# Kernel tuning notes

Hardware: AMD Instinct MI355X
Metric: run time of the kernel (lower is better)

The kernel has to match this reference:

```python
import jax, jax.numpy as jnp
import numpy as np
import math

B, S, H = 2, 2048, 2048
NH, HD = 16, 128
THETA = 10000.0
NEG = -1e9


def make_rope_tables(seq_len, head_dim, theta):
    inv_freq = 1.0 / (theta ** (np.arange(0, head_dim, 2, dtype=np.float32) / head_dim))
    pos = np.arange(seq_len, dtype=np.float32)
    freqs = np.outer(pos, inv_freq)                    # (S, HD/2)
    emb = np.concatenate([freqs, freqs], axis=-1)      # (S, HD)
    return jnp.asarray(np.cos(emb)), jnp.asarray(np.sin(emb))


def setup_inputs() -> dict:
    key = jax.random.key(0)
    k1, k2, k3 = jax.random.split(key, 3)
    hidden_states = jax.random.normal(k1, (B, S, H), dtype=jnp.float32)
    rope_cos, rope_sin = make_rope_tables(S, HD, THETA)
    # additive causal mask [1,1,S,S]
    causal = jnp.tril(jnp.ones((S, S), dtype=bool))
    attention_mask = jnp.where(causal, 0.0, NEG).astype(jnp.float32)[None, None]
    w_qkv = jax.random.normal(k2, (3 * H, H), dtype=jnp.float32) * (1.0 / math.sqrt(H))
    w_o = jax.random.normal(k3, (H, H), dtype=jnp.float32) * (1.0 / math.sqrt(H))
    return {"hidden_states": hidden_states, "rope_cos": rope_cos, "rope_sin": rope_sin,
            "attention_mask": attention_mask, "w_qkv": w_qkv, "w_o": w_o}


def apply_rope(x, cos, sin):
    # x: (B, NH, S, HD); cos/sin: (S, HD)
    half = x.shape[-1] // 2
    x1, x2 = x[..., :half], x[..., half:]
    x_rot = jnp.concatenate([-x2, x1], axis=-1)
    return x * cos[None, None] + x_rot * sin[None, None]


def reference(hidden_states, rope_cos, rope_sin, attention_mask, w_qkv, w_o):
    b, s, h = hidden_states.shape
    qkv = hidden_states @ w_qkv.T                      # (B, S, 3H)
    qkv = qkv.reshape(b, s, 3, NH, HD).transpose(2, 0, 3, 1, 4)  # (3, B, NH, S, HD)
    q, k, v = qkv[0], qkv[1], qkv[2]
    q = apply_rope(q, rope_cos, rope_sin)
    k = apply_rope(k, rope_cos, rope_sin)
    scale = 1.0 / math.sqrt(HD)
    scores = jnp.einsum('bhqd,bhkd->bhqk', q, k) * scale + attention_mask
    probs = jax.nn.softmax(scores.astype(jnp.float32), axis=-1).astype(q.dtype)
    out = jnp.einsum('bhqk,bhkd->bhqd', probs, v)      # (B, NH, S, HD)
    out = out.transpose(0, 2, 1, 3).reshape(b, s, h)
    return out @ w_o.T
```

## Files before the change

kernel.cpp:

```cpp
#include <hip/hip_runtime.h>
#include <stdint.h>

typedef unsigned int u32;
typedef unsigned short u16;

typedef __bf16 bf16x8 __attribute__((ext_vector_type(8)));
typedef float f32x4 __attribute__((ext_vector_type(4)));

struct alignas(16) V16 { u32 a, b, c, d; };

__device__ __forceinline__ u16 f2bf(float x) {
    u32 u = __float_as_uint(x);
    u += 0x7FFFu + ((u >> 16) & 1u);
    return (u16)(u >> 16);
}
__device__ __forceinline__ float bf2f(u16 h) {
    return __uint_as_float(((u32)h) << 16);
}

__device__ __forceinline__ bf16x8 ld_frag(const u16* p) {
    return __builtin_bit_cast(bf16x8, *(const V16*)p);
}

__device__ __forceinline__ void async_cp16(u16* lds_dst, const u16* g_src) {
    __builtin_amdgcn_global_load_lds(
        (__attribute__((address_space(1))) void*)g_src,
        (__attribute__((address_space(3))) void*)lds_dst, 16, 0, 0);
}

__global__ __launch_bounds__(256) void cast_all_kernel(
    const float* __restrict__ hidden, const float* __restrict__ wqkv,
    const float* __restrict__ wo,
    u16* __restrict__ hA, u16* __restrict__ wqb, u16* __restrict__ wob)
{
    int i = blockIdx.x * 256 + threadIdx.x;
    const float* src; u16* dst; int off;
    if (i < 2097152)      { src = hidden; dst = hA;  off = i; }
    else if (i < 5242880) { src = wqkv;   dst = wqb; off = i - 2097152; }
    else                  { src = wo;     dst = wob; off = i - 5242880; }
    const float* p = src + (size_t)off * 4;
    ushort4 o;
    o.x = f2bf(p[0]); o.y = f2bf(p[1]); o.z = f2bf(p[2]); o.w = f2bf(p[3]);
    *(ushort4*)(dst + (size_t)off * 4) = o;
}

__global__ __launch_bounds__(256) void gemm_bt(
    const u16* __restrict__ A, const u16* __restrict__ Bt,
    int M, int N, int K, int mode,
    float* __restrict__ Cout,
    u16* __restrict__ Qb, u16* __restrict__ Kb, u16* __restrict__ Vtb)
{
    __shared__ u16 smem[17408];
    u16* As = smem;
    u16* Bs = smem + 8192;

    const int t = threadIdx.x;
    const int w = t >> 6, l = t & 63;
    const int lr = l & 15;
    const int lk = (l >> 4) * 8;

    const int flat = blockIdx.y * gridDim.x + blockIdx.x;
    const int xcd = flat & 7, slot = flat >> 3;
    const int cpx = gridDim.x >> 3;
    const int ncol = xcd * cpx + slot % cpx;
    const int mrow = slot / cpx;
    const int m0 = mrow * 128, n0 = ncol * 128;
    const int wm = (w >> 1) * 64, wn = (w & 1) * 64;

    f32x4 acc[4][4];
#pragma unroll
    for (int i = 0; i < 4; ++i)
#pragma unroll
        for (int j = 0; j < 4; ++j) acc[i][j] = f32x4{0.f, 0.f, 0.f, 0.f};

    const u16* Ag = A + (size_t)m0 * K;
    const u16* Bg = Bt + (size_t)n0 * K;
    const int srow = l >> 2;
    const int scol = (l & 3) * 8;

    for (int k0 = 0; k0 < K; k0 += 64) {
#pragma unroll
        for (int g = 0; g < 2; ++g) {
            const int row = w * 32 + g * 16;
#pragma unroll
            for (int c = 0; c < 2; ++c) {
                async_cp16(&As[c * 4096 + row * 32],
                           Ag + (size_t)(row + srow) * K + k0 + c * 32 + scol);
                async_cp16(&Bs[c * 4096 + row * 32],
                           Bg + (size_t)(row + srow) * K + k0 + c * 32 + scol);
            }
        }
        __syncthreads();

#pragma unroll
        for (int c = 0; c < 2; ++c) {
            bf16x8 af[4], bf[4];
#pragma unroll
            for (int i = 0; i < 4; ++i)
                af[i] = ld_frag(&As[c * 4096 + (wm + i * 16 + lr) * 32 + lk]);
#pragma unroll
            for (int j = 0; j < 4; ++j)
                bf[j] = ld_frag(&Bs[c * 4096 + (wn + j * 16 + lr) * 32 + lk]);
#pragma unroll
            for (int i = 0; i < 4; ++i)
#pragma unroll
                for (int j = 0; j < 4; ++j)
                    acc[i][j] = __builtin_amdgcn_mfma_f32_16x16x32_bf16(af[i], bf[j], acc[i][j], 0, 0, 0);
        }
        __syncthreads();
    }

    const int lrow4 = (l >> 4) * 4;
    if (mode == 1) {
#pragma unroll
        for (int i = 0; i < 4; ++i)
#pragma unroll
            for (int j = 0; j < 4; ++j)
#pragma unroll
                for (int r = 0; r < 4; ++r) {
                    int gr = m0 + wm + i * 16 + lrow4 + r;
                    int gc = n0 + wn + j * 16 + lr;
                    Cout[(size_t)gr * N + gc] = acc[i][j][r];
                }
    } else {
        const int which = n0 >> 11;
        const int nh = (n0 & 2047) >> 7;
        const int bb = m0 >> 11;
        const int s0 = m0 & 2047;
        u16* Cs = smem;
        if (which < 2) {
#pragma unroll
            for (int i = 0; i < 4; ++i)
#pragma unroll
                for (int j = 0; j < 4; ++j)
#pragma unroll
                    for (int r = 0; r < 4; ++r)
                        Cs[(wm + i * 16 + lrow4 + r) * 136 + wn + j * 16 + lr] =
                            f2bf(acc[i][j][r]);
        } else {
#pragma unroll
            for (int i = 0; i < 4; ++i)
#pragma unroll
                for (int j = 0; j < 4; ++j)
#pragma unroll
                    for (int r = 0; r < 4; ++r)
                        Cs[(wn + j * 16 + lr) * 136 + wm + i * 16 + lrow4 + r] =
                            f2bf(acc[i][j][r]);
        }
        __syncthreads();
        const int rrow = t >> 4, rcol = (t & 15) * 8;
        if (which < 2) {
            u16* dst = (which == 0 ? Qb : Kb) +
                       ((size_t)(bb * 16 + nh) * 2048 + s0) * 128;
#pragma unroll
            for (int it = 0; it < 8; ++it) {
                int row = it * 16 + rrow;
                *(V16*)&dst[(size_t)row * 128 + rcol] = *(const V16*)&Cs[row * 136 + rcol];
            }
        } else {
            u16* dst = Vtb + (size_t)(bb * 16 + nh) * 128 * 2048 + s0;
#pragma unroll
            for (int it = 0; it < 8; ++it) {
                int d = it * 16 + rrow;
                *(V16*)&dst[(size_t)d * 2048 + rcol] = *(const V16*)&Cs[d * 136 + rcol];
            }
        }
    }
}

__global__ __launch_bounds__(256) void rope_kernel(
    u16* __restrict__ Qb, u16* __restrict__ Kb,
    const float* __restrict__ cosT, const float* __restrict__ sinT, float qscale)
{
    int idx = blockIdx.x * 256 + threadIdx.x;
    int d = (idx & 7) * 8;
    int s = (idx >> 3) & 2047;
    int bh = idx >> 14;
    size_t base = ((size_t)bh * 2048 + s) * 128;
    float c[8], sn[8];
#pragma unroll
    for (int i = 0; i < 8; ++i) {
        c[i]  = cosT[s * 128 + d + i];
        sn[i] = sinT[s * 128 + d + i];
    }
    union U { V16 v; u16 h[8]; };
    U qlo, qhi, klo, khi, a, bq, ak, bk;
    qlo.v = *(const V16*)&Qb[base + d];
    qhi.v = *(const V16*)&Qb[base + d + 64];
    klo.v = *(const V16*)&Kb[base + d];
    khi.v = *(const V16*)&Kb[base + d + 64];
#pragma unroll
    for (int i = 0; i < 8; ++i) {
        float q1 = bf2f(qlo.h[i]), q2 = bf2f(qhi.h[i]);
        a.h[i]  = f2bf((q1 * c[i] - q2 * sn[i]) * qscale);
        bq.h[i] = f2bf((q2 * c[i] + q1 * sn[i]) * qscale);
        float k1 = bf2f(klo.h[i]), k2 = bf2f(khi.h[i]);
        ak.h[i] = f2bf(k1 * c[i] - k2 * sn[i]);
        bk.h[i] = f2bf(k2 * c[i] + k1 * sn[i]);
    }
    *(V16*)&Qb[base + d]      = a.v;
    *(V16*)&Qb[base + d + 64] = bq.v;
    *(V16*)&Kb[base + d]      = ak.v;
    *(V16*)&Kb[base + d + 64] = bk.v;
}

#define PS_LD 72
__global__ __launch_bounds__(256, 2) void flash_attn(
    const u16* __restrict__ Qb, const u16* __restrict__ Kb, const u16* __restrict__ Vtb,
    u16* __restrict__ ctx)
{
    __shared__ u16 Ks[4 * 64 * 32];
    __shared__ u16 Vts[2 * 128 * 32];
    __shared__ u16 Ps[4 * 16 * PS_LD];

    const int t = threadIdx.x, w = t >> 6, l = t & 63;
    const int lr = l & 15, lk = (l >> 4) * 8, lrow4 = (l >> 4) * 4;
    const int bh = blockIdx.x;
    const int pidx = blockIdx.y;
    const int wm = w * 16;

    const u16* Qg = Qb + (size_t)bh * 2048 * 128;
    const u16* Kg = Kb + (size_t)bh * 2048 * 128;
    const u16* Vg = Vtb + (size_t)bh * 128 * 2048;
    u16* Pw = &Ps[w * 16 * PS_LD];

    const int srow = l >> 2;
    const int scol = (l & 3) * 8;
    const int vh = w & 1, vkc = w >> 1;

    const int b = bh >> 4, nh = bh & 15;

#pragma unroll
    for (int half = 0; half < 2; ++half) {
        const int qt = half ? pidx : 31 - pidx;
        const int q0 = qt * 64;

        bf16x8 qfrag[4];
#pragma unroll
        for (int kc = 0; kc < 4; ++kc)
            qfrag[kc] = ld_frag(&Qg[(size_t)(q0 + wm + lr) * 128 + kc * 32 + lk]);

        f32x4 oacc[8];
#pragma unroll
        for (int jo = 0; jo < 8; ++jo) oacc[jo] = f32x4{0.f, 0.f, 0.f, 0.f};
        float l_part[4] = {0.f, 0.f, 0.f, 0.f};

        const int ktiles = qt + 1;
        for (int kt = 0; kt < ktiles; ++kt) {
            const int c0 = kt * 64;
#pragma unroll
            for (int it = 0; it < 4; ++it)
                async_cp16(&Ks[w * 2048 + it * 512],
                           Kg + (size_t)(c0 + it * 16 + srow) * 128 + w * 32 + scol);
#pragma unroll
            for (int it = 0; it < 4; ++it)
                async_cp16(&Vts[vkc * 4096 + (vh * 64 + it * 16) * 32],
                           Vg + (size_t)(vh * 64 + it * 16 + srow) * 2048 + c0 + vkc * 32 + scol);
            __syncthreads();

            f32x4 pacc[4];
#pragma unroll
            for (int j = 0; j < 4; ++j) pacc[j] = f32x4{0.f, 0.f, 0.f, 0.f};
#pragma unroll
            for (int kc = 0; kc < 4; ++kc) {
                bf16x8 bk[4];
#pragma unroll
                for (int j = 0; j < 4; ++j)
                    bk[j] = ld_frag(&Ks[kc * 2048 + (j * 16 + lr) * 32 + lk]);
#pragma unroll
                for (int j = 0; j < 4; ++j)
                    pacc[j] = __builtin_amdgcn_mfma_f32_16x16x32_bf16(qfrag[kc], bk[j], pacc[j], 0, 0, 0);
            }

            if (kt == qt) {
#pragma unroll
                for (int j = 0; j < 4; ++j) {
                    const int cl = j * 16 + lr;
#pragma unroll
                    for (int r = 0; r < 4; ++r) {
                        float pv = (cl > wm + lrow4 + r) ? 0.f : __expf(pacc[j][r]);
                        pacc[j][r] = pv;
                        l_part[r] += pv;
                    }
                }
            } else {
#pragma unroll
                for (int j = 0; j < 4; ++j)
#pragma unroll
                    for (int r = 0; r < 4; ++r) {
                        float pv = __expf(pacc[j][r]);
                        pacc[j][r] = pv;
                        l_part[r] += pv;
                    }
            }

#pragma unroll
            for (int j = 0; j < 4; ++j)
#pragma unroll
                for (int r = 0; r < 4; ++r)
                    Pw[(lrow4 + r) * PS_LD + j * 16 + lr] = f2bf(pacc[j][r]);

#pragma unroll
            for (int kc = 0; kc < 2; ++kc) {
                bf16x8 ap = ld_frag(&Pw[lr * PS_LD + kc * 32 + lk]);
#pragma unroll
                for (int jo = 0; jo < 8; ++jo) {
                    bf16x8 bv = ld_frag(&Vts[kc * 4096 + (jo * 16 + lr) * 32 + lk]);
                    oacc[jo] = __builtin_amdgcn_mfma_f32_16x16x32_bf16(ap, bv, oacc[jo], 0, 0, 0);
                }
            }
            __syncthreads();
        }

        float linv[4];
#pragma unroll
        for (int r = 0; r < 4; ++r) {
            float s = l_part[r];
#pragma unroll
            for (int dd = 8; dd >= 1; dd >>= 1) s += __shfl_xor(s, dd);
            linv[r] = __builtin_amdgcn_rcpf(s);
        }
#pragma unroll
        for (int jo = 0; jo < 8; ++jo)
#pragma unroll
            for (int r = 0; r < 4; ++r) {
                int srow2 = q0 + wm + lrow4 + r;
                int col = nh * 128 + jo * 16 + lr;
                ctx[((size_t)b * 2048 + srow2) * 2048 + col] = f2bf(oacc[jo][r] * linv[r]);
            }
    }
}

extern "C" void kernel_launch(void* const* d_in, const int* in_sizes, int n_in,
                              void* d_out, int out_size, void* d_ws, size_t ws_size,
                              hipStream_t stream)
{
    (void)in_sizes; (void)n_in; (void)out_size; (void)ws_size;
    const float* hidden = (const float*)d_in[0];
    const float* cosT   = (const float*)d_in[1];
    const float* sinT   = (const float*)d_in[2];
    const float* wqkv   = (const float*)d_in[4];
    const float* wo     = (const float*)d_in[5];
    float* out = (float*)d_out;
    char* ws = (char*)d_ws;

    u16* hA   = (u16*)(ws + 0);
    u16* wqb  = (u16*)(ws + 16777216);
    u16* wob  = (u16*)(ws + 41943040);
    u16* Qb   = (u16*)(ws + 50331648);
    u16* Kb   = (u16*)(ws + 67108864);
    u16* Vtb  = (u16*)(ws + 83886080);
    u16* ctx  = (u16*)(ws + 100663296);

    cast_all_kernel<<<dim3(24576), dim3(256), 0, stream>>>(hidden, wqkv, wo,
                                                           hA, wqb, wob);

    gemm_bt<<<dim3(48, 32), dim3(256), 0, stream>>>(hA, wqb, 4096, 6144, 2048, 0,
                                                    nullptr, Qb, Kb, Vtb);
    rope_kernel<<<dim3(2048), dim3(256), 0, stream>>>(Qb, Kb, cosT, sinT,
                                                      0.08838834764831845f);

    flash_attn<<<dim3(32, 16), dim3(256), 0, stream>>>(Qb, Kb, Vtb, ctx);

    gemm_bt<<<dim3(16, 32), dim3(256), 0, stream>>>(ctx, wob, 4096, 2048, 2048, 1,
                                                    out, nullptr, nullptr, nullptr);
}
```

Measured before the change: 398.6 us.

## Pipeline GEMMs with double-buffered LDS, fuse RoPE epilogue, swizzle attention LDS

Replaces the GEMM with a 512-thread, 256x128-tile kernel. It double-buffers half-K LDS stages and overlaps async global loads with MFMA work using vmcnt waits, raw barriers and setprio. LDS reads are XOR-swizzled to avoid bank conflicts. RoPE and the Q scale move into the QKV GEMM epilogue, which removes the separate rope kernel and its read-modify-write pass over Q and K. The flash attention K/V LDS layouts are also changed to swizzled full-row tiles. The cost is more LDS per block (96KB dynamic), hand-tuned waitcnt logic that is fragile, and fewer blocks for the output GEMM.

```diff
diff --git a/kernel.cpp b/kernel.cpp
--- a/kernel.cpp
+++ b/kernel.cpp
@@ -44,73 +44,141 @@
     *(ushort4*)(dst + (size_t)off * 4) = o;
 }
 
-__global__ __launch_bounds__(256) void gemm_bt(
+__device__ __forceinline__ void stage_A(
+    u16* smem, const u16* __restrict__ Ag, int K,
+    int kk, int buf, int tile, int w, int rg0, int chl)
+{
+    u16* base = smem + buf * 16384 + kk * 8192;
+    const int kcol = tile * 64 + kk * 32 + chl * 8;
+#pragma unroll
+    for (int i = 0; i < 2; ++i) {
+        const int s = i * 8 + w;
+        async_cp16(base + s * 512, Ag + (size_t)(s * 16 + rg0) * K + kcol);
+    }
+}
+__device__ __forceinline__ void stage_B(
+    u16* smem, const u16* __restrict__ Bg, int K,
+    int kk, int buf, int tile, int w, int rg0, int chl)
+{
+    u16* base = smem + 32768 + buf * 8192 + kk * 4096;
+    const int kcol = tile * 64 + kk * 32 + chl * 8;
+    async_cp16(base + w * 512, Bg + (size_t)(w * 16 + rg0) * K + kcol);
+}
+
+__global__ __launch_bounds__(512, 2) void gemm_mn(
     const u16* __restrict__ A, const u16* __restrict__ Bt,
     int M, int N, int K, int mode,
     float* __restrict__ Cout,
-    u16* __restrict__ Qb, u16* __restrict__ Kb, u16* __restrict__ Vtb)
-{
-    __shared__ u16 smem[17408];
-    u16* As = smem;
-    u16* Bs = smem + 8192;
-
+    u16* __restrict__ Qb, u16* __restrict__ Kb, u16* __restrict__ Vtb,
+    const float* __restrict__ cosT, const float* __restrict__ sinT, float qscale)
+{
+    extern __shared__ u16 smem[];
     const int t = threadIdx.x;
     const int w = t >> 6, l = t & 63;
-    const int lr = l & 15;
-    const int lk = (l >> 4) * 8;
+    const int lr = l & 15, lk = (l >> 4) * 8;
+    const int wmr = w >> 1, wnc = w & 1;
+    const int wmr4 = wmr * 4, wnc4 = wnc * 4;
+    const int laneoff = lr * 32 + (lk ^ ((lr & 8) ? 16 : 0));
+    const int rg0 = l >> 2;
+    const int chl = (l & 3) ^ ((l >> 4) & 2);
 
     const int flat = blockIdx.y * gridDim.x + blockIdx.x;
     const int xcd = flat & 7, slot = flat >> 3;
     const int cpx = gridDim.x >> 3;
     const int ncol = xcd * cpx + slot % cpx;
     const int mrow = slot / cpx;
-    const int m0 = mrow * 128, n0 = ncol * 128;
-    const int wm = (w >> 1) * 64, wn = (w & 1) * 64;
-
-    f32x4 acc[4][4];
-#pragma unroll
-    for (int i = 0; i < 4; ++i)
-#pragma unroll
-        for (int j = 0; j < 4; ++j) acc[i][j] = f32x4{0.f, 0.f, 0.f, 0.f};
+    const int m0 = mrow * 256, n0 = ncol * 128;
 
     const u16* Ag = A + (size_t)m0 * K;
     const u16* Bg = Bt + (size_t)n0 * K;
-    const int srow = l >> 2;
-    const int scol = (l & 3) * 8;
-
-    for (int k0 = 0; k0 < K; k0 += 64) {
-#pragma unroll
-        for (int g = 0; g < 2; ++g) {
-            const int row = w * 32 + g * 16;
-#pragma unroll
-            for (int c = 0; c < 2; ++c) {
-                async_cp16(&As[c * 4096 + row * 32],
-                           Ag + (size_t)(row + srow) * K + k0 + c * 32 + scol);
-                async_cp16(&Bs[c * 4096 + row * 32],
-                           Bg + (size_t)(row + srow) * K + k0 + c * 32 + scol);
-            }
-        }
-        __syncthreads();
-
-#pragma unroll
-        for (int c = 0; c < 2; ++c) {
-            bf16x8 af[4], bf[4];
+
+    f32x4 acc[4][4];
+#pragma unroll
+    for (int i = 0; i < 4; ++i)
+#pragma unroll
+        for (int j = 0; j < 4; ++j) acc[i][j] = f32x4{0.f, 0.f, 0.f, 0.f};
+
+    const int NT = K >> 6;
+
+    stage_A(smem, Ag, K, 0, 0, 0, w, rg0, chl);
+    stage_B(smem, Bg, K, 0, 0, 0, w, rg0, chl);
+    stage_A(smem, Ag, K, 1, 0, 0, w, rg0, chl);
+    stage_B(smem, Bg, K, 1, 0, 0, w, rg0, chl);
+    stage_A(smem, Ag, K, 0, 1, 1, w, rg0, chl);
+    stage_B(smem, Bg, K, 0, 1, 1, w, rg0, chl);
+    asm volatile("s_waitcnt vmcnt(6)" ::: "memory");
+    __builtin_amdgcn_s_barrier();
+
+    bf16x8 af0[4], bf0[4], af1[4], bf1[4];
+#pragma unroll
+    for (int i = 0; i < 4; ++i)
+        af0[i] = ld_frag(smem + (wmr4 + i) * 512 + laneoff);
+#pragma unroll
+    for (int j = 0; j < 4; ++j)
+        bf0[j] = ld_frag(smem + 32768 + (wnc4 + j) * 512 + laneoff);
+
+    for (int tt = 0; tt < NT; ++tt) {
+        const int bsel = tt & 1;
+        const u16* Ab  = smem + bsel * 16384;
+        const u16* Bb  = smem + 32768 + bsel * 8192;
+        const u16* AbN = smem + (bsel ^ 1) * 16384;
+        const u16* BbN = smem + 32768 + (bsel ^ 1) * 8192;
+
+        if (tt + 1 < NT) {
+            stage_A(smem, Ag, K, 1, bsel ^ 1, tt + 1, w, rg0, chl);
+            stage_B(smem, Bg, K, 1, bsel ^ 1, tt + 1, w, rg0, chl);
+        }
+        if (tt < NT - 1) asm volatile("s_waitcnt vmcnt(6)" ::: "memory");
+        else             asm volatile("s_waitcnt vmcnt(0)" ::: "memory");
+        __builtin_amdgcn_s_barrier();
+        __builtin_amdgcn_s_setprio(1);
+#pragma unroll
+        for (int i = 0; i < 4; ++i)
+            af1[i] = ld_frag(Ab + 8192 + (wmr4 + i) * 512 + laneoff);
+#pragma unroll
+        for (int j = 0; j < 4; ++j)
+            bf1[j] = ld_frag(Bb + 4096 + (wnc4 + j) * 512 + laneoff);
+        __builtin_amdgcn_sched_barrier(0);
+#pragma unroll
+        for (int i = 0; i < 4; ++i)
+#pragma unroll
+            for (int j = 0; j < 4; ++j)
+                acc[i][j] = __builtin_amdgcn_mfma_f32_16x16x32_bf16(
+                    af0[i], bf0[j], acc[i][j], 0, 0, 0);
+        __builtin_amdgcn_s_setprio(0);
+        __builtin_amdgcn_s_barrier();
+
+        if (tt + 2 < NT) {
+            stage_A(smem, Ag, K, 0, bsel, tt + 2, w, rg0, chl);
+            stage_B(smem, Bg, K, 0, bsel, tt + 2, w, rg0, chl);
+        }
+        if (tt < NT - 2)       asm volatile("s_waitcnt vmcnt(6)" ::: "memory");
+        else if (tt == NT - 2) asm volatile("s_waitcnt vmcnt(3)" ::: "memory");
+        __builtin_amdgcn_s_barrier();
+        __builtin_amdgcn_s_setprio(1);
+        if (tt + 1 < NT) {
 #pragma unroll
             for (int i = 0; i < 4; ++i)
-                af[i] = ld_frag(&As[c * 4096 + (wm + i * 16 + lr) * 32 + lk]);
-#pragma unroll
-            for (int j = 0; j < 4; ++j)
-                bf[j] = ld_frag(&Bs[c * 4096 + (wn + j * 16 + lr) * 32 + lk]);
-#pragma unroll
-            for (int i = 0; i < 4; ++i)
-#pragma unroll
-                for (int j = 0; j < 4; ++j)
-                    acc[i][j] = __builtin_amdgcn_mfma_f32_16x16x32_bf16(af[i], bf[j], acc[i][j], 0, 0, 0);
-        }
-        __syncthreads();
-    }
-
+                af0[i] = ld_frag(AbN + (wmr4 + i) * 512 + laneoff);
+#pragma unroll
+            for (int j = 0; j < 4; ++j)
+                bf0[j] = ld_frag(BbN + (wnc4 + j) * 512 + laneoff);
+        }
+        __builtin_amdgcn_sched_barrier(0);
+#pragma unroll
+        for (int i = 0; i < 4; ++i)
+#pragma unroll
+            for (int j = 0; j < 4; ++j)
+                acc[i][j] = __builtin_amdgcn_mfma_f32_16x16x32_bf16(
+                    af1[i], bf1[j], acc[i][j], 0, 0, 0);
+        __builtin_amdgcn_s_setprio(0);
+        __builtin_amdgcn_s_barrier();
+    }
+
+    __syncthreads();
     const int lrow4 = (l >> 4) * 4;
+    const int rb = wmr * 64, cb = wnc * 64;
+
     if (mode == 1) {
 #pragma unroll
         for (int i = 0; i < 4; ++i)
@@ -118,90 +186,71 @@
             for (int j = 0; j < 4; ++j)
 #pragma unroll
                 for (int r = 0; r < 4; ++r) {
-                    int gr = m0 + wm + i * 16 + lrow4 + r;
-                    int gc = n0 + wn + j * 16 + lr;
+                    int gr = m0 + rb + i * 16 + lrow4 + r;
+                    int gc = n0 + cb + j * 16 + lr;
                     Cout[(size_t)gr * N + gc] = acc[i][j][r];
                 }
+        return;
+    }
+
+    const int which = n0 >> 11;
+    const int nh = (n0 & 2047) >> 7;
+    const int bb = m0 >> 11;
+    const int s0 = m0 & 2047;
+
+    if (which < 2) {
+#pragma unroll
+        for (int i = 0; i < 4; ++i)
+#pragma unroll
+            for (int j = 0; j < 4; ++j)
+#pragma unroll
+                for (int r = 0; r < 4; ++r)
+                    smem[(rb + i * 16 + lrow4 + r) * 128 + cb + j * 16 + lr] =
+                        f2bf(acc[i][j][r]);
+        __syncthreads();
+        const bool isQ = (which == 0);
+        u16* dstb = isQ ? Qb : Kb;
+        const float qs = isQ ? qscale : 1.0f;
+#pragma unroll
+        for (int ps = 0; ps < 8; ++ps) {
+            int chunk = ps * 512 + t;
+            int row = chunk >> 4;
+            int ce = (chunk & 15) * 8;
+            union { V16 v; u16 h[8]; } xv, pv, ov;
+            xv.v = *(const V16*)&smem[row * 128 + ce];
+            pv.v = *(const V16*)&smem[row * 128 + (ce ^ 64)];
+            const float* cp = cosT + (size_t)(s0 + row) * 128 + ce;
+            const float* sp = sinT + (size_t)(s0 + row) * 128 + ce;
+            const float sgn = (ce < 64) ? -1.f : 1.f;
+#pragma unroll
+            for (int i = 0; i < 8; ++i) {
+                float x  = bf2f(xv.h[i]);
+                float xr = bf2f(pv.h[i]);
+                ov.h[i] = f2bf((x * cp[i] + sgn * xr * sp[i]) * qs);
+            }
+            *(V16*)&dstb[((size_t)(bb * 16 + nh) * 2048 + s0 + row) * 128 + ce] = ov.v;
+        }
     } else {
-        const int which = n0 >> 11;
-        const int nh = (n0 & 2047) >> 7;
-        const int bb = m0 >> 11;
-        const int s0 = m0 & 2047;
-        u16* Cs = smem;
-        if (which < 2) {
-#pragma unroll
-            for (int i = 0; i < 4; ++i)
-#pragma unroll
-                for (int j = 0; j < 4; ++j)
-#pragma unroll
-                    for (int r = 0; r < 4; ++r)
-                        Cs[(wm + i * 16 + lrow4 + r) * 136 + wn + j * 16 + lr] =
-                            f2bf(acc[i][j][r]);
-        } else {
-#pragma unroll
-            for (int i = 0; i < 4; ++i)
-#pragma unroll
-                for (int j = 0; j < 4; ++j)
-#pragma unroll
-                    for (int r = 0; r < 4; ++r)
-                        Cs[(wn + j * 16 + lr) * 136 + wm + i * 16 + lrow4 + r] =
-                            f2bf(acc[i][j][r]);
-        }
+#pragma unroll
+        for (int i = 0; i < 4; ++i)
+#pragma unroll
+            for (int j = 0; j < 4; ++j)
+#pragma unroll
+                for (int r = 0; r < 4; ++r) {
+                    int cr = cb + j * 16 + lr;
+                    int cc = rb + i * 16 + lrow4 + r;
+                    smem[cr * 256 + (cc ^ ((cr & 7) << 3))] = f2bf(acc[i][j][r]);
+                }
         __syncthreads();
-        const int rrow = t >> 4, rcol = (t & 15) * 8;
-        if (which < 2) {
-            u16* dst = (which == 0 ? Qb : Kb) +
-                       ((size_t)(bb * 16 + nh) * 2048 + s0) * 128;
-#pragma unroll
-            for (int it = 0; it < 8; ++it) {
-                int row = it * 16 + rrow;
-                *(V16*)&dst[(size_t)row * 128 + rcol] = *(const V16*)&Cs[row * 136 + rcol];
-            }
-        } else {
-            u16* dst = Vtb + (size_t)(bb * 16 + nh) * 128 * 2048 + s0;
-#pragma unroll
-            for (int it = 0; it < 8; ++it) {
-                int d = it * 16 + rrow;
-                *(V16*)&dst[(size_t)d * 2048 + rcol] = *(const V16*)&Cs[d * 136 + rcol];
-            }
-        }
-    }
-}
-
-__global__ __launch_bounds__(256) void rope_kernel(
-    u16* __restrict__ Qb, u16* __restrict__ Kb,
-    const float* __restrict__ cosT, const float* __restrict__ sinT, float qscale)
-{
-    int idx = blockIdx.x * 256 + threadIdx.x;
-    int d = (idx & 7) * 8;
-    int s = (idx >> 3) & 2047;
-    int bh = idx >> 14;
-    size_t base = ((size_t)bh * 2048 + s) * 128;
-    float c[8], sn[8];
-#pragma unroll
-    for (int i = 0; i < 8; ++i) {
-        c[i]  = cosT[s * 128 + d + i];
-        sn[i] = sinT[s * 128 + d + i];
-    }
-    union U { V16 v; u16 h[8]; };
-    U qlo, qhi, klo, khi, a, bq, ak, bk;
-    qlo.v = *(const V16*)&Qb[base + d];
-    qhi.v = *(const V16*)&Qb[base + d + 64];
-    klo.v = *(const V16*)&Kb[base + d];
-    khi.v = *(const V16*)&Kb[base + d + 64];
-#pragma unroll
-    for (int i = 0; i < 8; ++i) {
-        float q1 = bf2f(qlo.h[i]), q2 = bf2f(qhi.h[i]);
-        a.h[i]  = f2bf((q1 * c[i] - q2 * sn[i]) * qscale);
-        bq.h[i] = f2bf((q2 * c[i] + q1 * sn[i]) * qscale);
-        float k1 = bf2f(klo.h[i]), k2 = bf2f(khi.h[i]);
-        ak.h[i] = f2bf(k1 * c[i] - k2 * sn[i]);
-        bk.h[i] = f2bf(k2 * c[i] + k1 * sn[i]);
-    }
-    *(V16*)&Qb[base + d]      = a.v;
-    *(V16*)&Qb[base + d + 64] = bq.v;
-    *(V16*)&Kb[base + d]      = ak.v;
-    *(V16*)&Kb[base + d + 64] = bk.v;
+#pragma unroll
+        for (int ps = 0; ps < 8; ++ps) {
+            int chunk = ps * 512 + t;
+            int drow = chunk >> 5;
+            int se = (chunk & 31) * 8;
+            *(V16*)&Vtb[((size_t)(bb * 16 + nh) * 128 + drow) * 2048 + s0 + se] =
+                *(const V16*)&smem[drow * 256 + (se ^ ((drow & 7) << 3))];
+        }
+    }
 }
 
 #define PS_LD 72
@@ -209,12 +258,14 @@
     const u16* __restrict__ Qb, const u16* __restrict__ Kb, const u16* __restrict__ Vtb,
     u16* __restrict__ ctx)
 {
-    __shared__ u16 Ks[4 * 64 * 32];
-    __shared__ u16 Vts[2 * 128 * 32];
+    __shared__ u16 Ks[64 * 128];
+    __shared__ u16 Vts[128 * 64];
     __shared__ u16 Ps[4 * 16 * PS_LD];
 
     const int t = threadIdx.x, w = t >> 6, l = t & 63;
     const int lr = l & 15, lk = (l >> 4) * 8, lrow4 = (l >> 4) * 4;
+    const int hi = l >> 4;
+    const int xw = lr & 7;
     const int bh = blockIdx.x;
     const int pidx = blockIdx.y;
     const int wm = w * 16;
@@ -224,9 +275,9 @@
     const u16* Vg = Vtb + (size_t)bh * 128 * 2048;
     u16* Pw = &Ps[w * 16 * PS_LD];
 
-    const int srow = l >> 2;
-    const int scol = (l & 3) * 8;
-    const int vh = w & 1, vkc = w >> 1;
+    const int krow_l = l >> 4;
+    const int vrow_l = l >> 3;
+    const int vchk = ((l & 7) ^ vrow_l) * 8;
 
     const int b = bh >> 4, nh = bh & 15;
 
@@ -249,13 +300,18 @@
         for (int kt = 0; kt < ktiles; ++kt) {
             const int c0 = kt * 64;
 #pragma unroll
-            for (int it = 0; it < 4; ++it)
+            for (int it = 0; it < 4; ++it) {
+                const int krow = it * 4 + krow_l;
+                const int kchk = ((l & 15) ^ (krow & 7)) * 8;
                 async_cp16(&Ks[w * 2048 + it * 512],
-                           Kg + (size_t)(c0 + it * 16 + srow) * 128 + w * 32 + scol);
-#pragma unroll
-            for (int it = 0; it < 4; ++it)
-                async_cp16(&Vts[vkc * 4096 + (vh * 64 + it * 16) * 32],
-                           Vg + (size_t)(vh * 64 + it * 16 + srow) * 2048 + c0 + vkc * 32 + scol);
+                           Kg + (size_t)(c0 + w * 16 + krow) * 128 + kchk);
+            }
+#pragma unroll
+            for (int it = 0; it < 4; ++it) {
+                const int vrow = w * 32 + it * 8 + vrow_l;
+                async_cp16(&Vts[w * 2048 + it * 512],
+                           Vg + (size_t)vrow * 2048 + c0 + vchk);
+            }
             __syncthreads();
 
             f32x4 pacc[4];
@@ -263,10 +319,11 @@
             for (int j = 0; j < 4; ++j) pacc[j] = f32x4{0.f, 0.f, 0.f, 0.f};
 #pragma unroll
             for (int kc = 0; kc < 4; ++kc) {
+                const int kco = ((kc * 4 + hi) ^ xw) * 8;
                 bf16x8 bk[4];
 #pragma unroll
                 for (int j = 0; j < 4; ++j)
-                    bk[j] = ld_frag(&Ks[kc * 2048 + (j * 16 + lr) * 32 + lk]);
+                    bk[j] = ld_frag(&Ks[(j * 16 + lr) * 128 + kco]);
 #pragma unroll
                 for (int j = 0; j < 4; ++j)
                     pacc[j] = __builtin_amdgcn_mfma_f32_16x16x32_bf16(qfrag[kc], bk[j], pacc[j], 0, 0, 0);
@@ -303,9 +360,10 @@
 #pragma unroll
             for (int kc = 0; kc < 2; ++kc) {
                 bf16x8 ap = ld_frag(&Pw[lr * PS_LD + kc * 32 + lk]);
+                const int vco = ((kc * 4 + hi) ^ xw) * 8;
 #pragma unroll
                 for (int jo = 0; jo < 8; ++jo) {
-                    bf16x8 bv = ld_frag(&Vts[kc * 4096 + (jo * 16 + lr) * 32 + lk]);
+                    bf16x8 bv = ld_frag(&Vts[(jo * 16 + lr) * 64 + vco]);
                     oacc[jo] = __builtin_amdgcn_mfma_f32_16x16x32_bf16(ap, bv, oacc[jo], 0, 0, 0);
                 }
             }
@@ -352,16 +410,23 @@
     u16* Vtb  = (u16*)(ws + 83886080);
     u16* ctx  = (u16*)(ws + 100663296);
 
+    static bool attr_done = false;
+    if (!attr_done) {
+        hipFuncSetAttribute((const void*)gemm_mn,
+                            hipFuncAttributeMaxDynamicSharedMemorySize, 98304);
+        attr_done = true;
+    }
+
     cast_all_kernel<<<dim3(24576), dim3(256), 0, stream>>>(hidden, wqkv, wo,
                                                            hA, wqb, wob);
 
-    gemm_bt<<<dim3(48, 32), dim3(256), 0, stream>>>(hA, wqb, 4096, 6144, 2048, 0,
-                                                    nullptr, Qb, Kb, Vtb);
-    rope_kernel<<<dim3(2048), dim3(256), 0, stream>>>(Qb, Kb, cosT, sinT,
-                                                      0.08838834764831845f);
+    gemm_mn<<<dim3(48, 16), dim3(512), 98304, stream>>>(
+        hA, wqb, 4096, 6144, 2048, 0, nullptr, Qb, Kb, Vtb,
+        cosT, sinT, 0.08838834764831845f);
 
     flash_attn<<<dim3(32, 16), dim3(256), 0, stream>>>(Qb, Kb, Vtb, ctx);
 
-    gemm_bt<<<dim3(16, 32), dim3(256), 0, stream>>>(ctx, wob, 4096, 2048, 2048, 1,
-                                                    out, nullptr, nullptr, nullptr);
-}
+    gemm_mn<<<dim3(16, 16), dim3(512), 98304, stream>>>(
+        ctx, wob, 4096, 2048, 2048, 1, out, nullptr, nullptr, nullptr,
+        nullptr, nullptr, 0.f);
+}
```

New measurement: 377.2 us. -5.4%, faster.
